# Optimization experiments

Measured on AMD Instinct MI355X. Metric: run time of the kernel, lower is better.

Reference implementation:

```python
import jax, jax.numpy as jnp
import numpy as np

NB_FEATURES = 128
ACCUMULATION = 4


def iterative_inv(mat, n_iter=6):
    # Newton-Schulz iteration for matrix inverse ('original' init: global max)
    I = jnp.eye(mat.shape[-1], dtype=mat.dtype)
    K = mat
    V = (1.0 / jnp.max(jnp.sum(K, axis=-2))) * jnp.swapaxes(K, -1, -2)
    for _ in range(n_iter):
        KV = K @ V
        V = 0.25 * V @ (13.0 * I - KV @ (15.0 * I - KV @ (7.0 * I - KV)))
    return V


def setup_inputs() -> dict:
    key = jax.random.key(0)
    kq, kk, kv, ks = jax.random.split(key, 4)
    b, h, n, d = 4, 8, 2048, 64
    q = jax.random.normal(kq, (b, h, n, d), dtype=jnp.float32)
    k = jax.random.normal(kk, (b, h, n, d), dtype=jnp.float32)
    v = jax.random.normal(kv, (b, h, n, d), dtype=jnp.float32)
    mask = jnp.ones((b, n), dtype=jnp.float32)
    total = ACCUMULATION * NB_FEATURES
    # uniform_sketching: indices in [0,n) scaled by non_padding_num (=n here),
    # second half of the flat index list offset by +n to index the k-block of X.
    S = jax.random.randint(ks, (b, total), 0, n)
    S = S.at[:, total // 2:].add(n)
    sketching_matrix = S.reshape(b, ACCUMULATION, NB_FEATURES)
    random_sign = jnp.ones((b, ACCUMULATION, NB_FEATURES), dtype=jnp.float32)
    return {"q": q, "k": k, "v": v, "mask": mask,
            "random_sign": random_sign, "sketching_matrix": sketching_matrix}


def reference(q, k, v, mask, random_sign, sketching_matrix):
    b, h, n, d = q.shape
    data_normalizer = 32.0 ** (-0.25)
    m = mask[:, None, :, None]                      # [b,1,n,1]
    q = q * (m * data_normalizer)
    k = k * (m * data_normalizer)
    v = v * m

    X = jnp.concatenate([q, k], axis=2)             # [b,h,2n,d]
    Xt = jnp.transpose(X, (0, 2, 1, 3))             # [b,2n,h,d]
    XS = Xt[jnp.arange(b)[:, None, None], sketching_matrix]  # [b,acc,f,h,d]
    XS = jnp.transpose(XS, (0, 3, 1, 2, 4))         # [b,h,acc,f,d]

    # RS-RBF kernel sketch: exp(x.y - |x|^2/2 - |y|^2/2), accumulated over acc
    diag1 = (0.5 * jnp.sum(X * X, axis=-1))[:, :, None, :, None]   # [b,h,1,2n,1]
    diag2 = (0.5 * jnp.sum(XS * XS, axis=-1))[:, :, :, None, :]    # [b,h,acc,1,f]
    prod = jnp.einsum('bhnp,bhmfp->bhmnf', X, XS) - diag1 - diag2  # [b,h,acc,2n,f]
    res = jnp.exp(prod)
    res = jnp.transpose(res, (0, 1, 3, 2, 4))       # [b,h,2n,acc,f]
    AS = jnp.einsum('bhnmf,bmf->bhnf', res, random_sign)  # [b,h,2n,f]

    Q = AS[:, :, :n]                                # [b,h,n,f]
    K = AS[:, :, n:]                                # [b,h,n,f]

    ASt = jnp.transpose(AS, (0, 2, 1, 3))           # [b,2n,h,f]
    STAS = ASt[jnp.arange(b)[:, None, None], sketching_matrix]     # [b,acc,f,h,f]
    STAS = jnp.einsum('bmdhe,bmd->bhde', STAS, random_sign)        # [b,h,f,f]
    f = STAS.shape[-1]
    STAS = STAS + 0.1 * jnp.eye(f, dtype=STAS.dtype)

    D_inv = jnp.sqrt(1.0 / jnp.sum(STAS, axis=-1))  # [b,h,f]
    STAS_n = D_inv[..., :, None] * STAS * D_inv[..., None, :]
    STAS_inv = iterative_inv(STAS_n, 6)

    K = (K * D_inv[:, :, None, :]) @ STAS_inv       # [b,h,n,f]
    K = K * D_inv[:, :, None, :] * m

    context = jnp.einsum('bhnf,bhne->bhfe', K, v)   # [b,h,f,d]
    out = Q @ context                               # [b,h,n,d]
    return out
```

## Files before the change

kernel.cpp:

```cpp
#include <hip/hip_runtime.h>

constexpr int Bc = 4, Hc = 8, Nc = 2048, Dc = 64, Fc = 128, Mc = 4;
constexpr int BHc = Bc*Hc;
constexpr int T2c = 2*Nc;
constexpr int Jc  = Mc*Fc;
constexpr float DNORM = 0.4204482076268573f;

constexpr size_t OFF_AS    = 0;
constexpr size_t OFF_XSH   = OFF_AS    + (size_t)BHc*T2c*Fc;
constexpr size_t OFF_XSM   = OFF_XSH   + (size_t)BHc*Jc*Dc/2;
constexpr size_t OFF_XSL   = OFF_XSM   + (size_t)BHc*Jc*Dc/2;
constexpr size_t OFF_DIAG1 = OFF_XSL   + (size_t)BHc*Jc*Dc/2;
constexpr size_t OFF_DIAG2 = OFF_DIAG1 + (size_t)BHc*T2c;
constexpr size_t OFF_STASN = OFF_DIAG2 + (size_t)BHc*Jc;
constexpr size_t OFF_VBUF  = OFF_STASN + (size_t)BHc*Fc*Fc;
constexpr size_t OFF_DINV  = OFF_VBUF  + (size_t)BHc*Fc*Fc;
constexpr size_t OFF_GMAX  = OFF_DINV  + (size_t)BHc*Fc;
constexpr size_t OFF_CTX   = OFF_GMAX  + 64;
constexpr size_t OFF_KH    = OFF_CTX   + (size_t)BHc*Fc*Dc;
constexpr size_t OFF_KM    = OFF_KH    + (size_t)BHc*Fc*Fc/2;
constexpr size_t OFF_KL    = OFF_KM    + (size_t)BHc*Fc*Fc/2;
constexpr size_t OFF_GPART = OFF_XSH;

typedef __attribute__((ext_vector_type(8))) short bf16x8;
typedef __attribute__((ext_vector_type(4))) float f32x4;
typedef __attribute__((ext_vector_type(4))) unsigned short u16x4;

__device__ __forceinline__ unsigned short f2bf_rne(float x) {
  unsigned int u = __float_as_uint(x);
  u += 0x7fff + ((u >> 16) & 1);
  return (unsigned short)(u >> 16);
}
__device__ __forceinline__ float bf2f(unsigned short h) {
  return __uint_as_float(((unsigned int)h) << 16);
}

__global__ __launch_bounds__(256) void diag1_kernel(
    const float* __restrict__ q, const float* __restrict__ k,
    const float* __restrict__ mask, float* __restrict__ diag1) {
  int gid = blockIdx.x*256 + threadIdx.x;
  int kq  = gid & 15;
  int row = gid >> 4;
  int t   = row & (T2c - 1);
  int bh  = row >> 12;
  int b   = bh >> 3;
  int tn  = (t < Nc) ? t : t - Nc;
  const float* src = ((t < Nc) ? q : k) + ((size_t)bh*Nc + tn)*Dc;
  float sc = DNORM * mask[b*Nc + tn];
  float4 x = *(const float4*)(src + kq*4);
  float s = x.x*x.x + x.y*x.y + x.z*x.z + x.w*x.w;
  s += __shfl_xor(s, 1);
  s += __shfl_xor(s, 2);
  s += __shfl_xor(s, 4);
  s += __shfl_xor(s, 8);
  if (kq == 0) diag1[row] = 0.5f * sc * sc * s;
}

__global__ __launch_bounds__(256) void gather_kernel(
    const float* __restrict__ q, const float* __restrict__ k,
    const float* __restrict__ mask, const int* __restrict__ sketch,
    const float* __restrict__ diag1,
    unsigned short* __restrict__ xsh, unsigned short* __restrict__ xsm,
    unsigned short* __restrict__ xsl, float* __restrict__ diag2) {
  int gid = blockIdx.x*256 + threadIdx.x;
  int kq  = gid & 15;
  int idx = gid >> 4;
  int j   = idx & (Jc - 1);
  int bh  = idx >> 9;
  int b   = bh >> 3;
  int t   = sketch[b*Jc + j];
  int tn  = (t < Nc) ? t : t - Nc;
  const float* src = ((t < Nc) ? q : k) + ((size_t)bh*Nc + tn)*Dc;
  float sc = DNORM * mask[b*Nc + tn];
  float4 x = *(const float4*)(src + kq*4);
  float xv[4] = {x.x*sc, x.y*sc, x.z*sc, x.w*sc};
  u16x4 hh, mm_, ll;
  #pragma unroll
  for (int jj = 0; jj < 4; ++jj) {
    unsigned short h = f2bf_rne(xv[jj]);
    float r1 = xv[jj] - bf2f(h);
    unsigned short m = f2bf_rne(r1);
    float r2 = r1 - bf2f(m);
    hh[jj] = h; mm_[jj] = m; ll[jj] = f2bf_rne(r2);
  }
  *(u16x4*)(xsh + (size_t)idx*Dc + kq*4) = hh;
  *(u16x4*)(xsm + (size_t)idx*Dc + kq*4) = mm_;
  *(u16x4*)(xsl + (size_t)idx*Dc + kq*4) = ll;
  if (kq == 0) diag2[idx] = diag1[bh*T2c + t];
}

__global__ __launch_bounds__(256) void as_mfma_kernel(
    const float* __restrict__ q, const float* __restrict__ k,
    const float* __restrict__ mask,
    const unsigned short* __restrict__ xsh, const unsigned short* __restrict__ xsm,
    const unsigned short* __restrict__ xsl,
    const float* __restrict__ diag1, const float* __restrict__ diag2,
    const float* __restrict__ sign, float* __restrict__ AS) {
  __shared__ __align__(16) unsigned short Ah[64][72];
  __shared__ __align__(16) unsigned short Am[64][72];
  __shared__ __align__(16) unsigned short Al[64][72];
  __shared__ float d1s[64];
  __shared__ float d2s[4][128];
  __shared__ float sgs[4][128];
  int bh = blockIdx.y, b = bh >> 3;
  int t0 = blockIdx.x * 64;
  int tid = threadIdx.x;
  int lane = tid & 63, wid = tid >> 6;
  int wr = wid >> 1, wc = wid & 1;
  int l16 = lane & 15, lg = lane >> 4;
  int R0 = wr*32, C0 = wc*64;

  for (int i = tid; i < 64*16; i += 256) {
    int r = i >> 4, kq = i & 15;
    int t = t0 + r;
    int tn = (t < Nc) ? t : t - Nc;
    const float* src = ((t < Nc) ? q : k) + ((size_t)bh*Nc + tn)*Dc + kq*4;
    float sc = DNORM * mask[b*Nc + tn];
    float4 x = *(const float4*)src;
    float xv[4] = {x.x*sc, x.y*sc, x.z*sc, x.w*sc};
    u16x4 hv, mv, lv;
    #pragma unroll
    for (int jj = 0; jj < 4; ++jj) {
      unsigned short h = f2bf_rne(xv[jj]);
      float r1 = xv[jj] - bf2f(h);
      unsigned short m = f2bf_rne(r1);
      float r2 = r1 - bf2f(m);
      hv[jj] = h; mv[jj] = m; lv[jj] = f2bf_rne(r2);
    }
    *(u16x4*)&Ah[r][kq*4] = hv;
    *(u16x4*)&Am[r][kq*4] = mv;
    *(u16x4*)&Al[r][kq*4] = lv;
  }
  if (tid < 64) d1s[tid] = diag1[bh*T2c + t0 + tid];
  for (int i = tid; i < 512; i += 256) {
    d2s[i>>7][i&127] = diag2[bh*Jc + i];
    sgs[i>>7][i&127] = sign[b*Jc + i];
  }
  __syncthreads();

  const unsigned short* xhh = xsh + (size_t)bh*Jc*Dc;
  const unsigned short* xmm = xsm + (size_t)bh*Jc*Dc;
  const unsigned short* xll = xsl + (size_t)bh*Jc*Dc;
  f32x4 oa[2][4];
  #pragma unroll
  for (int m = 0; m < 2; ++m)
    #pragma unroll
    for (int n = 0; n < 4; ++n) oa[m][n] = 0.f;

  for (int m = 0; m < Mc; ++m) {
    f32x4 acc[2][4];
    #pragma unroll
    for (int mm = 0; mm < 2; ++mm)
      #pragma unroll
      for (int nn = 0; nn < 4; ++nn) acc[mm][nn] = 0.f;
    #pragma unroll
    for (int kc = 0; kc < Dc; kc += 32) {
      int ko = kc + lg*8;
      bf16x8 ah[2], am2[2], al2[2], bhv[4], bmv[4], blv[4];
      #pragma unroll
      for (int mm = 0; mm < 2; ++mm) {
        ah[mm]  = *(const bf16x8*)&Ah[R0+16*mm+l16][ko];
        am2[mm] = *(const bf16x8*)&Am[R0+16*mm+l16][ko];
        al2[mm] = *(const bf16x8*)&Al[R0+16*mm+l16][ko];
      }
      #pragma unroll
      for (int nn = 0; nn < 4; ++nn) {
        size_t p = (size_t)(m*Fc + C0 + 16*nn + l16)*Dc + ko;
        bhv[nn] = *(const bf16x8*)(xhh + p);
        bmv[nn] = *(const bf16x8*)(xmm + p);
        blv[nn] = *(const bf16x8*)(xll + p);
      }
      #pragma unroll
      for (int mm = 0; mm < 2; ++mm)
        #pragma unroll
        for (int nn = 0; nn < 4; ++nn) {
          acc[mm][nn] = __builtin_amdgcn_mfma_f32_16x16x32_bf16(am2[mm], bmv[nn], acc[mm][nn], 0,0,0);
          acc[mm][nn] = __builtin_amdgcn_mfma_f32_16x16x32_bf16(ah[mm],  blv[nn], acc[mm][nn], 0,0,0);
          acc[mm][nn] = __builtin_amdgcn_mfma_f32_16x16x32_bf16(al2[mm], bhv[nn], acc[mm][nn], 0,0,0);
          acc[mm][nn] = __builtin_amdgcn_mfma_f32_16x16x32_bf16(ah[mm],  bmv[nn], acc[mm][nn], 0,0,0);
          acc[mm][nn] = __builtin_amdgcn_mfma_f32_16x16x32_bf16(am2[mm], bhv[nn], acc[mm][nn], 0,0,0);
          acc[mm][nn] = __builtin_amdgcn_mfma_f32_16x16x32_bf16(ah[mm],  bhv[nn], acc[mm][nn], 0,0,0);
        }
    }
    #pragma unroll
    for (int mm = 0; mm < 2; ++mm)
      #pragma unroll
      for (int nn = 0; nn < 4; ++nn) {
        int c = C0 + 16*nn + l16;
        float d2v = d2s[m][c], sg = sgs[m][c];
        #pragma unroll
        for (int r = 0; r < 4; ++r) {
          int row = R0 + 16*mm + 4*lg + r;
          oa[mm][nn][r] += sg * __expf(acc[mm][nn][r] - d1s[row] - d2v);
        }
      }
  }
  #pragma unroll
  for (int mm = 0; mm < 2; ++mm)
    #pragma unroll
    for (int nn = 0; nn < 4; ++nn) {
      int c = C0 + 16*nn + l16;
      #pragma unroll
      for (int r = 0; r < 4; ++r) {
        int row = R0 + 16*mm + 4*lg + r;
        AS[((size_t)bh*T2c + t0 + row)*Fc + c] = oa[mm][nn][r];
      }
    }
}

__global__ __launch_bounds__(256) void stas_kernel(
    const float* __restrict__ AS, const int* __restrict__ sketch,
    const float* __restrict__ sign,
    float* __restrict__ STASn, float* __restrict__ Dinv,
    unsigned short* __restrict__ Kh, unsigned short* __restrict__ Km,
    unsigned short* __restrict__ Kl,
    unsigned int* __restrict__ gmax) {
  extern __shared__ float stas[];
  __shared__ int   Ssh[Jc];
  __shared__ float sgn[Jc];
  __shared__ float Dl[Fc];
  __shared__ float red[Fc];
  int bh = blockIdx.x;
  int b  = bh >> 3;
  int tid = threadIdx.x;
  for (int i = tid; i < Jc; i += 256) {
    Ssh[i] = sketch[b*Jc + i];
    sgn[i] = sign[b*Jc + i];
  }
  __syncthreads();
  for (int i = tid; i < Fc*Fc; i += 256) {
    int dd = i >> 7, e = i & 127;
    float vsum = 0.f;
    #pragma unroll
    for (int m = 0; m < Mc; ++m) {
      int t = Ssh[m*Fc + dd];
      vsum += sgn[m*Fc + dd] * AS[((size_t)bh*T2c + t)*Fc + e];
    }
    if (dd == e) vsum += 0.1f;
    stas[dd*129 + e] = vsum;
  }
  __syncthreads();
  if (tid < Fc) {
    float s = 0.f;
    for (int e = 0; e < Fc; ++e) s += stas[tid*129 + e];
    float di = 1.0f / sqrtf(s);
    Dl[tid] = di;
    Dinv[bh*Fc + tid] = di;
  }
  __syncthreads();
  for (int i = tid; i < Fc*Fc; i += 256) {
    int dd = i >> 7, e = i & 127;
    float vv = stas[dd*129 + e] * Dl[dd] * Dl[e];
    stas[dd*129 + e] = vv;
    STASn[(size_t)bh*Fc*Fc + i] = vv;
    unsigned short hb = f2bf_rne(vv); float r1 = vv - bf2f(hb);
    unsigned short mb = f2bf_rne(r1); float r2 = r1 - bf2f(mb);
    Kh[(size_t)bh*Fc*Fc + i] = hb;
    Km[(size_t)bh*Fc*Fc + i] = mb;
    Kl[(size_t)bh*Fc*Fc + i] = f2bf_rne(r2);
  }
  __syncthreads();
  if (tid < Fc) {
    float s = 0.f;
    for (int dd = 0; dd < Fc; ++dd) s += stas[dd*129 + tid];
    red[tid] = s;
  }
  __syncthreads();
  if (tid == 0) {
    float mx = 0.f;
    for (int e = 0; e < Fc; ++e) mx = fmaxf(mx, red[e]);
    atomicMax(gmax, __float_as_uint(mx));
  }
}

__device__ __forceinline__ unsigned aoff(int brow, int ke) {
  unsigned byte = ((unsigned)brow << 9) | ((unsigned)ke << 2);
  return byte ^ (((unsigned)(brow & 7)) << 4);
}
__device__ __forceinline__ unsigned boff(int brow, int ke) {
  unsigned byte = ((unsigned)brow << 8) | ((unsigned)ke << 1);
  return byte ^ (((unsigned)(brow & 7)) << 4);
}

__device__ __forceinline__ void split8(const f32x4& a, const f32x4& b,
                                       bf16x8& h, bf16x8& m, bf16x8& l) {
  float t[8] = {a[0],a[1],a[2],a[3],b[0],b[1],b[2],b[3]};
  #pragma unroll
  for (int j = 0; j < 8; ++j) {
    float x = t[j];
    unsigned short hb = f2bf_rne(x);
    float r1 = x - bf2f(hb);
    unsigned short mb = f2bf_rne(r1);
    float r2 = r1 - bf2f(mb);
    h[j] = (short)hb; m[j] = (short)mb; l[j] = (short)f2bf_rne(r2);
  }
}

__device__ __forceinline__ void ld_splitA(const char* Af, int brow, int ko,
                                          bf16x8& h, bf16x8& m, bf16x8& l) {
  f32x4 a = *(const f32x4*)(Af + aoff(brow, ko));
  f32x4 b = *(const f32x4*)(Af + aoff(brow, ko + 4));
  split8(a, b, h, m, l);
}

__device__ __forceinline__ void mm6(const bf16x8 ah[2], const bf16x8 am[2], const bf16x8 al[2],
                                    const bf16x8 bh[4], const bf16x8 bm[4], const bf16x8 bl[4],
                                    f32x4 acc[2][4]) {
  #pragma unroll
  for (int m = 0; m < 2; ++m)
    #pragma unroll
    for (int n = 0; n < 4; ++n) {
      acc[m][n] = __builtin_amdgcn_mfma_f32_16x16x32_bf16(am[m], bm[n], acc[m][n], 0,0,0);
      acc[m][n] = __builtin_amdgcn_mfma_f32_16x16x32_bf16(ah[m], bl[n], acc[m][n], 0,0,0);
      acc[m][n] = __builtin_amdgcn_mfma_f32_16x16x32_bf16(al[m], bh[n], acc[m][n], 0,0,0);
      acc[m][n] = __builtin_amdgcn_mfma_f32_16x16x32_bf16(ah[m], bm[n], acc[m][n], 0,0,0);
      acc[m][n] = __builtin_amdgcn_mfma_f32_16x16x32_bf16(am[m], bh[n], acc[m][n], 0,0,0);
      acc[m][n] = __builtin_amdgcn_mfma_f32_16x16x32_bf16(ah[m], bh[n], acc[m][n], 0,0,0);
    }
}

__device__ __forceinline__ void mm_p1(
    const unsigned short* __restrict__ kh, const unsigned short* __restrict__ km,
    const unsigned short* __restrict__ kl, const char* Af,
    int R0, int C0, int l16, int lg, f32x4 acc[2][4]) {
  #pragma unroll 1
  for (int kc = 0; kc < Fc; kc += 32) {
    int ko = kc + lg*8;
    bf16x8 ah[2], am[2], al[2], bh[4], bm[4], bl[4];
    #pragma unroll
    for (int m = 0; m < 2; ++m) {
      size_t p = (size_t)(R0+16*m+l16)*Fc + ko;
      ah[m] = *(const bf16x8*)(kh + p);
      am[m] = *(const bf16x8*)(km + p);
      al[m] = *(const bf16x8*)(kl + p);
    }
    #pragma unroll
    for (int n = 0; n < 4; ++n)
      ld_splitA(Af, C0+16*n+l16, ko, bh[n], bm[n], bl[n]);
    mm6(ah, am, al, bh, bm, bl, acc);
  }
}

__device__ __forceinline__ void mm_ldsB(const char* Af,
    const char* Zh, const char* Zm, const char* Zl,
    int R0, int C0, int l16, int lg, f32x4 acc[2][4]) {
  #pragma unroll 1
  for (int kc = 0; kc < Fc; kc += 32) {
    int ko = kc + lg*8;
    bf16x8 ah[2], am[2], al[2], bh[4], bm[4], bl[4];
    #pragma unroll
    for (int m = 0; m < 2; ++m)
      ld_splitA(Af, R0+16*m+l16, ko, ah[m], am[m], al[m]);
    #pragma unroll
    for (int n = 0; n < 4; ++n) {
      unsigned off = boff(C0+16*n+l16, ko);
      bh[n] = *(const bf16x8*)(Zh + off);
      bm[n] = *(const bf16x8*)(Zm + off);
      bl[n] = *(const bf16x8*)(Zl + off);
    }
    mm6(ah, am, al, bh, bm, bl, acc);
  }
}

__device__ __forceinline__ void wbA(char* Af, int col, int row0, f32x4 v) {
  *(f32x4*)(Af + aoff(col, row0)) = v;
}
__device__ __forceinline__ void wbZ(char* Zh, char* Zm, char* Zl,
                                    int col, int row0, f32x4 v) {
  u16x4 hv, mv, lv;
  #pragma unroll
  for (int r = 0; r < 4; ++r) {
    unsigned short hb = f2bf_rne(v[r]); float r1 = v[r] - bf2f(hb);
    unsigned short mb = f2bf_rne(r1);   float r2 = r1 - bf2f(mb);
    hv[r] = hb; mv[r] = mb; lv[r] = f2bf_rne(r2);
  }
  unsigned off = boff(col, row0);
  *(u16x4*)(Zh + off) = hv;
  *(u16x4*)(Zm + off) = mv;
  *(u16x4*)(Zl + off) = lv;
}

__global__ __launch_bounds__(512) void newton_ctx_kernel(
    const float* __restrict__ STASn,
    const unsigned short* __restrict__ KhG, const unsigned short* __restrict__ KmG,
    const unsigned short* __restrict__ KlG,
    const float* __restrict__ gmaxf, float* __restrict__ Vout,
    const float* __restrict__ ASg, const float* __restrict__ vg,
    const float* __restrict__ maskg, float* __restrict__ Gpart) {
  extern __shared__ char smc[];
  int tid  = threadIdx.x;

  if (blockIdx.x < BHc) {
    char* Zh = smc;
    char* Zm = smc + 32768;
    char* Zl = smc + 65536;
    char* Af = smc + 98304;
    int bh = blockIdx.x;
    const float* Kp = STASn + (size_t)bh*Fc*Fc;
    const unsigned short* kh = KhG + (size_t)bh*Fc*Fc;
    const unsigned short* km = KmG + (size_t)bh*Fc*Fc;
    const unsigned short* kl = KlG + (size_t)bh*Fc*Fc;
    float ginv = 1.0f / gmaxf[0];
    int lane = tid & 63;
    int wid  = tid >> 6;
    int wr = wid >> 1, wc = wid & 1;
    int l16 = lane & 15, lg = lane >> 4;
    int R0 = wr*32, C0 = wc*64;
    int drow0 = lg*4;

    f32x4 vreg[2][4];
    #pragma unroll
    for (int m = 0; m < 2; ++m)
      #pragma unroll
      for (int n = 0; n < 4; ++n) {
        int col = C0 + 16*n + l16;
        #pragma unroll
        for (int r = 0; r < 4; ++r)
          vreg[m][n][r] = Kp[(size_t)(R0 + 16*m + drow0 + r)*Fc + col] * ginv;
        wbA(Af, col, R0 + 16*m + drow0, vreg[m][n]);
      }
    __syncthreads();

    f32x4 fin[2][4];
    for (int it = 0; it < 6; ++it) {
      f32x4 acc[2][4];
      #pragma unroll
      for (int m = 0; m < 2; ++m) for (int n = 0; n < 4; ++n) acc[m][n] = 0.f;
      mm_p1(kh, km, kl, Af, R0, C0, l16, lg, acc);
      #pragma unroll
      for (int m = 0; m < 2; ++m)
        #pragma unroll
        for (int n = 0; n < 4; ++n)
          wbZ(Zh, Zm, Zl, C0 + 16*n + l16, R0 + 16*m + drow0, acc[m][n]);
      __syncthreads();

      #pragma unroll
      for (int m = 0; m < 2; ++m) for (int n = 0; n < 4; ++n) acc[m][n] = 0.f;
      mm_ldsB(Af, Zh, Zm, Zl, R0, C0, l16, lg, acc);
      #pragma unroll
      for (int m = 0; m < 2; ++m)
        #pragma unroll
        for (int n = 0; n < 4; ++n)
          fin[m][n] = 13.f*vreg[m][n] - 15.f*acc[m][n];
      __syncthreads();
      #pragma unroll
      for (int m = 0; m < 2; ++m)
        #pragma unroll
        for (int n = 0; n < 4; ++n)
          wbA(Af, C0 + 16*n + l16, R0 + 16*m + drow0, acc[m][n]);
      __syncthreads();

      #pragma unroll
      for (int m = 0; m < 2; ++m) for (int n = 0; n < 4; ++n) acc[m][n] = 0.f;
      mm_ldsB(Af, Zh, Zm, Zl, R0, C0, l16, lg, acc);
      #pragma unroll
      for (int m = 0; m < 2; ++m)
        #pragma unroll
        for (int n = 0; n < 4; ++n)
          fin[m][n] += 7.f*acc[m][n];
      __syncthreads();
      #pragma unroll
      for (int m = 0; m < 2; ++m)
        #pragma unroll
        for (int n = 0; n < 4; ++n)
          wbA(Af, C0 + 16*n + l16, R0 + 16*m + drow0, acc[m][n]);
      __syncthreads();

      #pragma unroll
      for (int m = 0; m < 2; ++m) for (int n = 0; n < 4; ++n) acc[m][n] = 0.f;
      mm_ldsB(Af, Zh, Zm, Zl, R0, C0, l16, lg, acc);
      #pragma unroll
      for (int m = 0; m < 2; ++m)
        #pragma unroll
        for (int n = 0; n < 4; ++n) {
          fin[m][n] = 0.25f*(fin[m][n] - acc[m][n]);
          vreg[m][n] = fin[m][n];
        }
      __syncthreads();
      #pragma unroll
      for (int m = 0; m < 2; ++m)
        #pragma unroll
        for (int n = 0; n < 4; ++n)
          wbA(Af, C0 + 16*n + l16, R0 + 16*m + drow0, fin[m][n]);
      __syncthreads();
    }

    float* Vo = Vout + (size_t)bh*Fc*Fc;
    #pragma unroll
    for (int m = 0; m < 2; ++m)
      #pragma unroll
      for (int n = 0; n < 4; ++n) {
        int col = C0 + 16*n + l16;
        #pragma unroll
        for (int r = 0; r < 4; ++r)
          Vo[(size_t)(R0 + 16*m + drow0 + r)*Fc + col] = vreg[m][n][r];
      }
  } else {
    float* Ksh = (float*)smc;
    float* vsh = (float*)(smc + 32768);
    int id = blockIdx.x - BHc;
    int cbh = id >> 2, chunk = id & 3;
    int cb = cbh >> 3;
    int t0 = chunk * 512;
    int f = tid & 127, g = tid >> 7;
    float acc[16];
    #pragma unroll
    for (int j = 0; j < 16; ++j) acc[j] = 0.f;
    for (int sub = 0; sub < 8; ++sub) {
      __syncthreads();
      int ts = t0 + sub*64;
      for (int i = tid; i < 64*32; i += 512) {
        int r = i >> 5, c4 = i & 31;
        *(float4*)&Ksh[r*128 + c4*4] =
            *(const float4*)(ASg + ((size_t)cbh*T2c + Nc + ts + r)*Fc + c4*4);
      }
      for (int i = tid; i < 64*16; i += 512) {
        int r = i >> 4, c4 = i & 15;
        float mk = maskg[cb*Nc + ts + r];
        float m2 = mk*mk;
        float4 x = *(const float4*)(vg + ((size_t)cbh*Nc + ts + r)*Dc + c4*4);
        x.x*=m2; x.y*=m2; x.z*=m2; x.w*=m2;
        *(float4*)&vsh[r*64 + c4*4] = x;
      }
      __syncthreads();
      #pragma unroll 2
      for (int tl = 0; tl < 64; ++tl) {
        float kf = Ksh[tl*128 + f];
        #pragma unroll
        for (int j4 = 0; j4 < 4; ++j4) {
          float4 vv = *(const float4*)&vsh[tl*64 + g*16 + j4*4];
          acc[j4*4+0] += kf*vv.x; acc[j4*4+1] += kf*vv.y;
          acc[j4*4+2] += kf*vv.z; acc[j4*4+3] += kf*vv.w;
        }
      }
    }
    float* gp = Gpart + ((((size_t)cbh*4 + chunk)*128 + f)*64 + g*16);
    #pragma unroll
    for (int j4 = 0; j4 < 4; ++j4)
      *(float4*)(gp + j4*4) = *(const float4*)&acc[j4*4];
  }
}

__global__ __launch_bounds__(256) void ctx_fix_kernel(
    const float* __restrict__ Gpart, const float* __restrict__ Vinv,
    const float* __restrict__ Dinv, float* __restrict__ ctxo) {
  __shared__ float DG[128*64];
  __shared__ float Dl[128];
  int bh = blockIdx.x;
  int tid = threadIdx.x;
  if (tid < 128) Dl[tid] = Dinv[bh*Fc + tid];
  __syncthreads();
  for (int i = tid; i < 2048; i += 256) {
    int e = i >> 4, c4 = i & 15;
    const float* g0 = Gpart + ((((size_t)bh*4)*128 + e)*64 + c4*4);
    float4 s0 = *(const float4*)(g0);
    float4 s1 = *(const float4*)(g0 + 8192);
    float4 s2 = *(const float4*)(g0 + 16384);
    float4 s3 = *(const float4*)(g0 + 24576);
    float de = Dl[e];
    float4 o;
    o.x = (s0.x+s1.x+s2.x+s3.x)*de;
    o.y = (s0.y+s1.y+s2.y+s3.y)*de;
    o.z = (s0.z+s1.z+s2.z+s3.z)*de;
    o.w = (s0.w+s1.w+s2.w+s3.w)*de;
    *(float4*)&DG[e*64 + c4*4] = o;
  }
  __syncthreads();
  int f = tid & 127, half = tid >> 7;
  float acc[32];
  #pragma unroll
  for (int j = 0; j < 32; ++j) acc[j] = 0.f;
  for (int e = 0; e < 128; ++e) {
    float s = Vinv[(size_t)bh*Fc*Fc + (size_t)e*Fc + f];
    #pragma unroll
    for (int j4 = 0; j4 < 8; ++j4) {
      float4 dg = *(const float4*)&DG[e*64 + half*32 + j4*4];
      acc[j4*4+0] += s*dg.x; acc[j4*4+1] += s*dg.y;
      acc[j4*4+2] += s*dg.z; acc[j4*4+3] += s*dg.w;
    }
  }
  float df = Dl[f];
  float* op = ctxo + (size_t)bh*Fc*Dc + f*Dc + half*32;
  #pragma unroll
  for (int j4 = 0; j4 < 8; ++j4) {
    float4 o;
    o.x = acc[j4*4+0]*df; o.y = acc[j4*4+1]*df;
    o.z = acc[j4*4+2]*df; o.w = acc[j4*4+3]*df;
    *(float4*)(op + j4*4) = o;
  }
}

__global__ __launch_bounds__(256) void out_kernel(
    const float* __restrict__ AS, const float* __restrict__ ctx,
    float* __restrict__ out) {
  extern __shared__ float smo[];
  float* Asq = smo;
  float* Cs  = smo + 64*132;
  int bh = blockIdx.y;
  int row0 = blockIdx.x * 64;
  int tid = threadIdx.x;
  int tr = tid >> 4, tc = tid & 15;
  for (int i = tid; i < 64*32; i += 256) {
    int r = i >> 5, kq = i & 31;
    *(float4*)&Asq[r*132 + kq*4] =
        *(const float4*)(AS + ((size_t)bh*T2c + row0 + r)*Fc + kq*4);
  }
  for (int i = tid; i < 128*16; i += 256) {
    int r = i >> 4, kq = i & 15;
    *(float4*)&Cs[r*64 + kq*4] =
        *(const float4*)(ctx + (size_t)bh*Fc*Dc + r*Dc + kq*4);
  }
  __syncthreads();
  float acc[4][4] = {};
  #pragma unroll 2
  for (int kk = 0; kk < Fc; ++kk) {
    float4 bv = *(const float4*)&Cs[kk*64 + tc*4];
    float a0 = Asq[(tr*4+0)*132 + kk];
    float a1 = Asq[(tr*4+1)*132 + kk];
    float a2 = Asq[(tr*4+2)*132 + kk];
    float a3 = Asq[(tr*4+3)*132 + kk];
    acc[0][0] += a0*bv.x; acc[0][1] += a0*bv.y; acc[0][2] += a0*bv.z; acc[0][3] += a0*bv.w;
    acc[1][0] += a1*bv.x; acc[1][1] += a1*bv.y; acc[1][2] += a1*bv.z; acc[1][3] += a1*bv.w;
    acc[2][0] += a2*bv.x; acc[2][1] += a2*bv.y; acc[2][2] += a2*bv.z; acc[2][3] += a2*bv.w;
    acc[3][0] += a3*bv.x; acc[3][1] += a3*bv.y; acc[3][2] += a3*bv.z; acc[3][3] += a3*bv.w;
  }
  #pragma unroll
  for (int i = 0; i < 4; ++i) {
    float4 o;
    o.x = acc[i][0]; o.y = acc[i][1]; o.z = acc[i][2]; o.w = acc[i][3];
    *(float4*)(out + ((size_t)bh*Nc + row0 + tr*4 + i)*Dc + tc*4) = o;
  }
}

extern "C" void kernel_launch(void* const* d_in, const int* in_sizes, int n_in,
                              void* d_out, int out_size, void* d_ws, size_t ws_size,
                              hipStream_t stream) {
  const float* q    = (const float*)d_in[0];
  const float* k    = (const float*)d_in[1];
  const float* v    = (const float*)d_in[2];
  const float* mask = (const float*)d_in[3];
  const float* sign = (const float*)d_in[4];
  const int*   sketch = (const int*)d_in[5];
  float* out = (float*)d_out;
  float* ws  = (float*)d_ws;

  unsigned short* xsh = (unsigned short*)(ws + OFF_XSH);
  unsigned short* xsm = (unsigned short*)(ws + OFF_XSM);
  unsigned short* xsl = (unsigned short*)(ws + OFF_XSL);
  unsigned short* kh  = (unsigned short*)(ws + OFF_KH);
  unsigned short* km  = (unsigned short*)(ws + OFF_KM);
  unsigned short* kl  = (unsigned short*)(ws + OFF_KL);

  hipMemsetAsync(ws + OFF_GMAX, 0, sizeof(float), stream);

  diag1_kernel<<<BHc*T2c*16/256, 256, 0, stream>>>(q, k, mask, ws + OFF_DIAG1);
  gather_kernel<<<BHc*Jc*16/256, 256, 0, stream>>>(q, k, mask, sketch, ws + OFF_DIAG1,
                                                   xsh, xsm, xsl, ws + OFF_DIAG2);
  as_mfma_kernel<<<dim3(T2c/64, BHc), 256, 0, stream>>>(q, k, mask, xsh, xsm, xsl,
      ws + OFF_DIAG1, ws + OFF_DIAG2, sign, ws + OFF_AS);
  stas_kernel<<<BHc, 256, 128*129*sizeof(float), stream>>>(ws + OFF_AS, sketch, sign,
      ws + OFF_STASN, ws + OFF_DINV, kh, km, kl, (unsigned int*)(ws + OFF_GMAX));
  newton_ctx_kernel<<<BHc + 128, 512, 163840, stream>>>(ws + OFF_STASN, kh, km, kl,
      ws + OFF_GMAX, ws + OFF_VBUF, ws + OFF_AS, v, mask, ws + OFF_GPART);
  ctx_fix_kernel<<<BHc, 256, 0, stream>>>(ws + OFF_GPART, ws + OFF_VBUF,
      ws + OFF_DINV, ws + OFF_CTX);
  out_kernel<<<dim3(Nc/64, BHc), 256, (64*132 + 128*64)*sizeof(float), stream>>>(
      ws + OFF_AS, ws + OFF_CTX, out);
}
```

Before: 379.4 us.

## Store Newton iterate pre-split into bf16 planes, spill low plane to global

The Newton-Schulz iterate is now stored in LDS as three pre-split bf16 planes (high, mid, low) instead of fp32. This removes the repeated fp32-to-bf16x3 split work in every matmul's inner loop. To fit the extra planes in the fixed LDS budget, the low-order plane of the intermediate Z is moved to a global scratch buffer and read from there. That trades LDS split ALU work for global-memory (likely L2-resident) traffic on the low plane.

```diff
diff --git a/kernel.cpp b/kernel.cpp
--- a/kernel.cpp
+++ b/kernel.cpp
@@ -21,6 +21,7 @@
 constexpr size_t OFF_KM    = OFF_KH    + (size_t)BHc*Fc*Fc/2;
 constexpr size_t OFF_KL    = OFF_KM    + (size_t)BHc*Fc*Fc/2;
 constexpr size_t OFF_GPART = OFF_XSH;
+constexpr size_t OFF_ZSC   = OFF_GPART + (size_t)BHc*4*128*64;
 
 typedef __attribute__((ext_vector_type(8))) short bf16x8;
 typedef __attribute__((ext_vector_type(4))) float f32x4;
@@ -273,34 +274,9 @@
   }
 }
 
-__device__ __forceinline__ unsigned aoff(int brow, int ke) {
-  unsigned byte = ((unsigned)brow << 9) | ((unsigned)ke << 2);
-  return byte ^ (((unsigned)(brow & 7)) << 4);
-}
 __device__ __forceinline__ unsigned boff(int brow, int ke) {
   unsigned byte = ((unsigned)brow << 8) | ((unsigned)ke << 1);
   return byte ^ (((unsigned)(brow & 7)) << 4);
-}
-
-__device__ __forceinline__ void split8(const f32x4& a, const f32x4& b,
-                                       bf16x8& h, bf16x8& m, bf16x8& l) {
-  float t[8] = {a[0],a[1],a[2],a[3],b[0],b[1],b[2],b[3]};
-  #pragma unroll
-  for (int j = 0; j < 8; ++j) {
-    float x = t[j];
-    unsigned short hb = f2bf_rne(x);
-    float r1 = x - bf2f(hb);
-    unsigned short mb = f2bf_rne(r1);
-    float r2 = r1 - bf2f(mb);
-    h[j] = (short)hb; m[j] = (short)mb; l[j] = (short)f2bf_rne(r2);
-  }
-}
-
-__device__ __forceinline__ void ld_splitA(const char* Af, int brow, int ko,
-                                          bf16x8& h, bf16x8& m, bf16x8& l) {
-  f32x4 a = *(const f32x4*)(Af + aoff(brow, ko));
-  f32x4 b = *(const f32x4*)(Af + aoff(brow, ko + 4));
-  split8(a, b, h, m, l);
 }
 
 __device__ __forceinline__ void mm6(const bf16x8 ah[2], const bf16x8 am[2], const bf16x8 al[2],
@@ -319,9 +295,18 @@
     }
 }
 
+__device__ __forceinline__ void ld3(const char* Ph, const char* Pm, const char* Pl,
+                                    int brow, int ko, bf16x8& h, bf16x8& m, bf16x8& l) {
+  unsigned off = boff(brow, ko);
+  h = *(const bf16x8*)(Ph + off);
+  m = *(const bf16x8*)(Pm + off);
+  l = *(const bf16x8*)(Pl + off);
+}
+
 __device__ __forceinline__ void mm_p1(
     const unsigned short* __restrict__ kh, const unsigned short* __restrict__ km,
-    const unsigned short* __restrict__ kl, const char* Af,
+    const unsigned short* __restrict__ kl,
+    const char* Ah, const char* Am, const char* Al,
     int R0, int C0, int l16, int lg, f32x4 acc[2][4]) {
   #pragma unroll 1
   for (int kc = 0; kc < Fc; kc += 32) {
@@ -336,13 +321,14 @@
     }
     #pragma unroll
     for (int n = 0; n < 4; ++n)
-      ld_splitA(Af, C0+16*n+l16, ko, bh[n], bm[n], bl[n]);
+      ld3(Ah, Am, Al, C0+16*n+l16, ko, bh[n], bm[n], bl[n]);
     mm6(ah, am, al, bh, bm, bl, acc);
   }
 }
 
-__device__ __forceinline__ void mm_ldsB(const char* Af,
-    const char* Zh, const char* Zm, const char* Zl,
+__device__ __forceinline__ void mm_p234(
+    const char* Ah, const char* Am, const char* Al,
+    const char* Zh, const char* Zm, const unsigned short* __restrict__ ZlG,
     int R0, int C0, int l16, int lg, f32x4 acc[2][4]) {
   #pragma unroll 1
   for (int kc = 0; kc < Fc; kc += 32) {
@@ -350,34 +336,44 @@
     bf16x8 ah[2], am[2], al[2], bh[4], bm[4], bl[4];
     #pragma unroll
     for (int m = 0; m < 2; ++m)
-      ld_splitA(Af, R0+16*m+l16, ko, ah[m], am[m], al[m]);
+      ld3(Ah, Am, Al, R0+16*m+l16, ko, ah[m], am[m], al[m]);
     #pragma unroll
     for (int n = 0; n < 4; ++n) {
-      unsigned off = boff(C0+16*n+l16, ko);
+      int col = C0+16*n+l16;
+      unsigned off = boff(col, ko);
       bh[n] = *(const bf16x8*)(Zh + off);
       bm[n] = *(const bf16x8*)(Zm + off);
-      bl[n] = *(const bf16x8*)(Zl + off);
+      bl[n] = *(const bf16x8*)(ZlG + col*Fc + ko);
     }
     mm6(ah, am, al, bh, bm, bl, acc);
   }
 }
 
-__device__ __forceinline__ void wbA(char* Af, int col, int row0, f32x4 v) {
-  *(f32x4*)(Af + aoff(col, row0)) = v;
-}
-__device__ __forceinline__ void wbZ(char* Zh, char* Zm, char* Zl,
-                                    int col, int row0, f32x4 v) {
-  u16x4 hv, mv, lv;
+__device__ __forceinline__ void split4(f32x4 v, u16x4& hv, u16x4& mv, u16x4& lv) {
   #pragma unroll
   for (int r = 0; r < 4; ++r) {
     unsigned short hb = f2bf_rne(v[r]); float r1 = v[r] - bf2f(hb);
     unsigned short mb = f2bf_rne(r1);   float r2 = r1 - bf2f(mb);
     hv[r] = hb; mv[r] = mb; lv[r] = f2bf_rne(r2);
   }
+}
+__device__ __forceinline__ void wbA3(char* Ah, char* Am, char* Al,
+                                     int col, int row0, f32x4 v) {
+  u16x4 hv, mv, lv;
+  split4(v, hv, mv, lv);
+  unsigned off = boff(col, row0);
+  *(u16x4*)(Ah + off) = hv;
+  *(u16x4*)(Am + off) = mv;
+  *(u16x4*)(Al + off) = lv;
+}
+__device__ __forceinline__ void wbZ3(char* Zh, char* Zm, unsigned short* __restrict__ ZlG,
+                                     int col, int row0, f32x4 v) {
+  u16x4 hv, mv, lv;
+  split4(v, hv, mv, lv);
   unsigned off = boff(col, row0);
   *(u16x4*)(Zh + off) = hv;
   *(u16x4*)(Zm + off) = mv;
-  *(u16x4*)(Zl + off) = lv;
+  *(u16x4*)(ZlG + col*Fc + row0) = lv;
 }
 
 __global__ __launch_bounds__(512) void newton_ctx_kernel(
@@ -386,20 +382,23 @@
     const unsigned short* __restrict__ KlG,
     const float* __restrict__ gmaxf, float* __restrict__ Vout,
     const float* __restrict__ ASg, const float* __restrict__ vg,
-    const float* __restrict__ maskg, float* __restrict__ Gpart) {
+    const float* __restrict__ maskg, float* __restrict__ Gpart,
+    unsigned short* __restrict__ ZlScr) {
   extern __shared__ char smc[];
   int tid  = threadIdx.x;
 
   if (blockIdx.x < BHc) {
-    char* Zh = smc;
-    char* Zm = smc + 32768;
-    char* Zl = smc + 65536;
-    char* Af = smc + 98304;
+    char* Ah = smc;
+    char* Am = smc + 32768;
+    char* Al = smc + 65536;
+    char* Zh = smc + 98304;
+    char* Zm = smc + 131072;
     int bh = blockIdx.x;
     const float* Kp = STASn + (size_t)bh*Fc*Fc;
     const unsigned short* kh = KhG + (size_t)bh*Fc*Fc;
     const unsigned short* km = KmG + (size_t)bh*Fc*Fc;
     const unsigned short* kl = KlG + (size_t)bh*Fc*Fc;
+    unsigned short* ZlG = ZlScr + (size_t)bh*Fc*Fc;
     float ginv = 1.0f / gmaxf[0];
     int lane = tid & 63;
     int wid  = tid >> 6;
@@ -417,7 +416,7 @@
         #pragma unroll
         for (int r = 0; r < 4; ++r)
           vreg[m][n][r] = Kp[(size_t)(R0 + 16*m + drow0 + r)*Fc + col] * ginv;
-        wbA(Af, col, R0 + 16*m + drow0, vreg[m][n]);
+        wbA3(Ah, Am, Al, col, R0 + 16*m + drow0, vreg[m][n]);
       }
     __syncthreads();
 
@@ -426,17 +425,17 @@
       f32x4 acc[2][4];
       #pragma unroll
       for (int m = 0; m < 2; ++m) for (int n = 0; n < 4; ++n) acc[m][n] = 0.f;
-      mm_p1(kh, km, kl, Af, R0, C0, l16, lg, acc);
+      mm_p1(kh, km, kl, Ah, Am, Al, R0, C0, l16, lg, acc);
       #pragma unroll
       for (int m = 0; m < 2; ++m)
         #pragma unroll
         for (int n = 0; n < 4; ++n)
-          wbZ(Zh, Zm, Zl, C0 + 16*n + l16, R0 + 16*m + drow0, acc[m][n]);
+          wbZ3(Zh, Zm, ZlG, C0 + 16*n + l16, R0 + 16*m + drow0, acc[m][n]);
       __syncthreads();
 
       #pragma unroll
       for (int m = 0; m < 2; ++m) for (int n = 0; n < 4; ++n) acc[m][n] = 0.f;
-      mm_ldsB(Af, Zh, Zm, Zl, R0, C0, l16, lg, acc);
+      mm_p234(Ah, Am, Al, Zh, Zm, ZlG, R0, C0, l16, lg, acc);
       #pragma unroll
       for (int m = 0; m < 2; ++m)
         #pragma unroll
@@ -447,12 +446,12 @@
       for (int m = 0; m < 2; ++m)
         #pragma unroll
         for (int n = 0; n < 4; ++n)
-          wbA(Af, C0 + 16*n + l16, R0 + 16*m + drow0, acc[m][n]);
+          wbA3(Ah, Am, Al, C0 + 16*n + l16, R0 + 16*m + drow0, acc[m][n]);
       __syncthreads();
 
       #pragma unroll
       for (int m = 0; m < 2; ++m) for (int n = 0; n < 4; ++n) acc[m][n] = 0.f;
-      mm_ldsB(Af, Zh, Zm, Zl, R0, C0, l16, lg, acc);
+      mm_p234(Ah, Am, Al, Zh, Zm, ZlG, R0, C0, l16, lg, acc);
       #pragma unroll
       for (int m = 0; m < 2; ++m)
         #pragma unroll
@@ -463,12 +462,12 @@
       for (int m = 0; m < 2; ++m)
         #pragma unroll
         for (int n = 0; n < 4; ++n)
-          wbA(Af, C0 + 16*n + l16, R0 + 16*m + drow0, acc[m][n]);
+          wbA3(Ah, Am, Al, C0 + 16*n + l16, R0 + 16*m + drow0, acc[m][n]);
       __syncthreads();
 
       #pragma unroll
       for (int m = 0; m < 2; ++m) for (int n = 0; n < 4; ++n) acc[m][n] = 0.f;
-      mm_ldsB(Af, Zh, Zm, Zl, R0, C0, l16, lg, acc);
+      mm_p234(Ah, Am, Al, Zh, Zm, ZlG, R0, C0, l16, lg, acc);
       #pragma unroll
       for (int m = 0; m < 2; ++m)
         #pragma unroll
@@ -481,7 +480,7 @@
       for (int m = 0; m < 2; ++m)
         #pragma unroll
         for (int n = 0; n < 4; ++n)
-          wbA(Af, C0 + 16*n + l16, R0 + 16*m + drow0, fin[m][n]);
+          wbA3(Ah, Am, Al, C0 + 16*n + l16, R0 + 16*m + drow0, fin[m][n]);
       __syncthreads();
     }
 
@@ -650,6 +649,7 @@
   unsigned short* kh  = (unsigned short*)(ws + OFF_KH);
   unsigned short* km  = (unsigned short*)(ws + OFF_KM);
   unsigned short* kl  = (unsigned short*)(ws + OFF_KL);
+  unsigned short* zsc = (unsigned short*)(ws + OFF_ZSC);
 
   hipMemsetAsync(ws + OFF_GMAX, 0, sizeof(float), stream);
 
@@ -661,7 +661,7 @@
   stas_kernel<<<BHc, 256, 128*129*sizeof(float), stream>>>(ws + OFF_AS, sketch, sign,
       ws + OFF_STASN, ws + OFF_DINV, kh, km, kl, (unsigned int*)(ws + OFF_GMAX));
   newton_ctx_kernel<<<BHc + 128, 512, 163840, stream>>>(ws + OFF_STASN, kh, km, kl,
-      ws + OFF_GMAX, ws + OFF_VBUF, ws + OFF_AS, v, mask, ws + OFF_GPART);
+      ws + OFF_GMAX, ws + OFF_VBUF, ws + OFF_AS, v, mask, ws + OFF_GPART, zsc);
   ctx_fix_kernel<<<BHc, 256, 0, stream>>>(ws + OFF_GPART, ws + OFF_VBUF,
       ws + OFF_DINV, ws + OFF_CTX);
   out_kernel<<<dim3(Nc/64, BHc), 256, (64*132 + 128*64)*sizeof(float), stream>>>(
```

Measured after the change: 359.6 us. 1.06x faster.
